# Kernel tuning notes

Hardware: AMD Instinct MI355X
Metric: run time of the kernel (lower is better)

Reference implementation:

```python
import jax, jax.numpy as jnp
import numpy as np

NUM_NEIGHBORS = 17
RATE = 0.5
BN_EPS = 1e-5
NEG_SLOPE = 0.1


def _neighbor_mask(n):
    # clamp branch (use_full_fov=False): mask[i, clamp(i+w, 0, n-1)] = 1 for w in [-k, k]
    half = NUM_NEIGHBORS // 2
    rows = np.arange(n)[:, None]
    cols = np.clip(rows + np.arange(-half, half + 1)[None, :], 0, n - 1)
    mask = np.zeros((n, n), dtype=np.float32)
    mask[np.repeat(np.arange(n), NUM_NEIGHBORS), cols.reshape(-1)] = 1.0
    return jnp.asarray(mask)


def _features(x, conv_w, conv_b, bn_gamma, bn_beta, bn_mean, bn_var):
    # conv kernel spans full length L with padding 0 -> a single dot per cutout
    # x: [B, N, C, L], conv_w: [H, C, L] -> [B, N, H]
    h = jnp.einsum('bncl,hcl->bnh', x, conv_w) + conv_b
    h = (h - bn_mean) * (bn_gamma / jnp.sqrt(bn_var + BN_EPS)) + bn_beta  # eval-mode BN1d
    return jnp.where(h >= 0, h, NEG_SLOPE * h)  # LeakyReLU(0.1)


def setup_inputs() -> dict:
    key = jax.random.key(0)
    ks = jax.random.split(key, 4)
    B, N, C, L, H = 8, 2048, 1, 56, 128
    return {
        'input': jax.random.normal(ks[0], (B, N, C, L), dtype=jnp.float32),
        'state_memory': jax.random.normal(ks[1], (B, N, C, L), dtype=jnp.float32),
        'conv_w': jax.random.normal(ks[2], (H, C, L), dtype=jnp.float32) * (2.0 / (C * L)) ** 0.5,
        'conv_b': jax.random.normal(ks[3], (H,), dtype=jnp.float32) * 0.02,
        'bn_gamma': jnp.ones((H,), dtype=jnp.float32),
        'bn_beta': jnp.zeros((H,), dtype=jnp.float32),
        'bn_mean': jnp.zeros((H,), dtype=jnp.float32),
        'bn_var': jnp.ones((H,), dtype=jnp.float32),
    }


def reference(input, state_memory, conv_w, conv_b, bn_gamma, bn_beta, bn_mean, bn_var):
    B, N, C, L = input.shape
    mask = _neighbor_mask(N)  # [N, N]

    f_in = _features(input, conv_w, conv_b, bn_gamma, bn_beta, bn_mean, bn_var)          # [B,N,H]
    f_mem = _features(state_memory, conv_w, conv_b, bn_gamma, bn_beta, bn_mean, bn_var)  # [B,N,H]

    sim = jnp.einsum('bnh,bmh->bnm', f_in, f_mem)      # [B,N,N]
    sim = sim - 1e10 * (1.0 - mask)
    sim_max = jnp.max(sim, axis=-1, keepdims=True)
    exps = jnp.exp(sim - sim_max) * mask
    attn = exps / jnp.sum(exps, axis=-1, keepdims=True)

    mem_flat = state_memory.reshape(B, N, C * L)
    attn_mem = jnp.einsum('bnm,bmd->bnd', attn, mem_flat).reshape(B, N, C, L)

    return RATE * input + (1.0 - RATE) * attn_mem
```

## Files before the change

### kernel.cpp

```cpp
#include <hip/hip_runtime.h>
#include <math.h>

#define NPTS   2048
#define LFEAT  56
#define HFEAT  128
#define HALFW  8
#define NEIGH  17
#define BR     32
#define BAND   48
#define LDW    132

__global__ __launch_bounds__(512) void fused_kernel(
    const float* __restrict__ x_in, const float* __restrict__ x_mem,
    const float* __restrict__ conv_w, const float* __restrict__ conv_b,
    const float* __restrict__ gamma,  const float* __restrict__ beta,
    const float* __restrict__ bmean,  const float* __restrict__ bvar,
    float* __restrict__ out, int R)
{
    __shared__ float4 xm4[BAND * 14];
    __shared__ float4 xi4[BR * 14];
    __shared__ float  fm[BAND][LDW];
    __shared__ float  fi[BR][LDW];

    const int tid    = threadIdx.x;
    const int chunks = NPTS / BR;
    const int b      = blockIdx.x / chunks;
    const int c0     = (blockIdx.x - b * chunks) * BR;
    const int bbase  = b * NPTS;

    const float4* srcm = (const float4*)(x_mem + (long)bbase * LFEAT);
    for (int i = tid; i < BAND * 14; i += 512) {
        const int r = i / 14, q = i - r * 14;
        const int g = min(max(c0 - HALFW + r, 0), NPTS - 1);
        xm4[i] = srcm[g * 14 + q];
    }
    const float4* srci = (const float4*)(x_in + (long)(bbase + c0) * LFEAT);
    for (int i = tid; i < BR * 14; i += 512) xi4[i] = srci[i];

    const int h  = tid & 127;
    const int rg = tid >> 7;
    float4 w4[14];
    #pragma unroll
    for (int q = 0; q < 14; ++q)
        w4[q] = ((const float4*)(conv_w + h * LFEAT))[q];
    const float sc = gamma[h] / sqrtf(bvar[h] + 1e-5f);
    const float sh = (conv_b[h] - bmean[h]) * sc + beta[h];

    __syncthreads();

    for (int r = rg; r < BAND; r += 4) {
        const float4* xr = &xm4[r * 14];
        float a0 = 0.0f, a1 = 0.0f;
        #pragma unroll
        for (int q = 0; q < 14; q += 2) {
            const float4 xa = xr[q], xb = xr[q + 1];
            a0 = fmaf(xa.x, w4[q].x, a0);     a0 = fmaf(xa.y, w4[q].y, a0);
            a0 = fmaf(xa.z, w4[q].z, a0);     a0 = fmaf(xa.w, w4[q].w, a0);
            a1 = fmaf(xb.x, w4[q + 1].x, a1); a1 = fmaf(xb.y, w4[q + 1].y, a1);
            a1 = fmaf(xb.z, w4[q + 1].z, a1); a1 = fmaf(xb.w, w4[q + 1].w, a1);
        }
        float f = (a0 + a1) * sc + sh;
        fm[r][h] = (f >= 0.0f) ? f : 0.1f * f;
    }
    for (int r = rg; r < BR; r += 4) {
        const float4* xr = &xi4[r * 14];
        float a0 = 0.0f, a1 = 0.0f;
        #pragma unroll
        for (int q = 0; q < 14; q += 2) {
            const float4 xa = xr[q], xb = xr[q + 1];
            a0 = fmaf(xa.x, w4[q].x, a0);     a0 = fmaf(xa.y, w4[q].y, a0);
            a0 = fmaf(xa.z, w4[q].z, a0);     a0 = fmaf(xa.w, w4[q].w, a0);
            a1 = fmaf(xb.x, w4[q + 1].x, a1); a1 = fmaf(xb.y, w4[q + 1].y, a1);
            a1 = fmaf(xb.z, w4[q + 1].z, a1); a1 = fmaf(xb.w, w4[q + 1].w, a1);
        }
        float f = (a0 + a1) * sc + sh;
        fi[r][h] = (f >= 0.0f) ? f : 0.1f * f;
    }
    __syncthreads();

    const int wave = tid >> 6;
    const int lane = tid & 63;
    const int lh   = lane & 31;
    const float* xmf = (const float*)xm4;
    const float* xif = (const float*)xi4;

    #pragma unroll
    for (int rr = 0; rr < 4; rr += 2) {
        const int l0   = wave * 4 + rr;
        const int lrow = l0 + (lane >> 5);
        const int n    = c0 + lrow;

        const int  mw    = n - HALFW + lh;
        const int  mc    = min(max(mw, 0), NPTS - 1);
        const int  slot  = mc - c0 + HALFW;
        const bool valid = (lh < NEIGH) && (mw >= 0) && (mw < NPTS);

        float p = -1e30f;
        if (lh < NEIGH) {
            const float4* a  = (const float4*)&fi[lrow][0];
            const float4* bb = (const float4*)&fm[slot][0];
            float4 A0 = {0.f,0.f,0.f,0.f}, A1 = {0.f,0.f,0.f,0.f};
            #pragma unroll
            for (int q = 0; q < 32; q += 2) {
                const float4 u0 = a[q],     v0 = bb[q];
                const float4 u1 = a[q + 1], v1 = bb[q + 1];
                A0.x = fmaf(u0.x, v0.x, A0.x); A0.y = fmaf(u0.y, v0.y, A0.y);
                A0.z = fmaf(u0.z, v0.z, A0.z); A0.w = fmaf(u0.w, v0.w, A0.w);
                A1.x = fmaf(u1.x, v1.x, A1.x); A1.y = fmaf(u1.y, v1.y, A1.y);
                A1.z = fmaf(u1.z, v1.z, A1.z); A1.w = fmaf(u1.w, v1.w, A1.w);
            }
            const float d = ((A0.x + A0.y) + (A0.z + A0.w))
                          + ((A1.x + A1.y) + (A1.z + A1.w));
            p = valid ? d : -1e30f;
        }

        float mx = p;
        #pragma unroll
        for (int off = 16; off >= 1; off >>= 1)
            mx = fmaxf(mx, __shfl_xor(mx, off));
        const float e = expf(p - mx);
        float sum = e;
        #pragma unroll
        for (int off = 16; off >= 1; off >>= 1)
            sum += __shfl_xor(sum, off);
        const float pn = e / sum;

        float swA[NEIGH], swB[NEIGH];
        #pragma unroll
        for (int w = 0; w < NEIGH; ++w) {
            swA[w] = __shfl(pn, w);
            swB[w] = __shfl(pn, 32 + w);
        }

        if (lane < LFEAT) {
            float accA = 0.0f, accB = 0.0f;
            #pragma unroll
            for (int w = 0; w < NEIGH; ++w) {
                const int sA = min(max(c0 + l0     - HALFW + w, 0), NPTS - 1) - c0 + HALFW;
                const int sB = min(max(c0 + l0 + 1 - HALFW + w, 0), NPTS - 1) - c0 + HALFW;
                accA = fmaf(swA[w], xmf[sA * LFEAT + lane], accA);
                accB = fmaf(swB[w], xmf[sB * LFEAT + lane], accB);
            }
            const long oA = (long)(bbase + c0 + l0) * LFEAT + lane;
            out[oA]         = 0.5f * xif[ l0      * LFEAT + lane] + 0.5f * accA;
            out[oA + LFEAT] = 0.5f * xif[(l0 + 1) * LFEAT + lane] + 0.5f * accB;
        }
    }
}

extern "C" void kernel_launch(void* const* d_in, const int* in_sizes, int n_in,
                              void* d_out, int out_size, void* d_ws, size_t ws_size,
                              hipStream_t stream)
{
    const float* input  = (const float*)d_in[0];
    const float* smem   = (const float*)d_in[1];
    const float* conv_w = (const float*)d_in[2];
    const float* conv_b = (const float*)d_in[3];
    const float* gamma  = (const float*)d_in[4];
    const float* beta   = (const float*)d_in[5];
    const float* bmean  = (const float*)d_in[6];
    const float* bvar   = (const float*)d_in[7];
    float* out = (float*)d_out;

    const int R = in_sizes[0] / LFEAT;
    const int blocks = (R / NPTS) * (NPTS / BR);

    fused_kernel<<<blocks, 512, 0, stream>>>(input, smem, conv_w, conv_b,
                                             gamma, beta, bmean, bvar, out, R);
}
```

Measured before the change: 101.4 us.

## Compute conv features from per-lane global loads broadcast with shuffles

The feature stage no longer reads the staged LDS rows. Each wave loads one 56-float row from global memory into lanes, prefetches the next row, and broadcasts elements with __shfl for the dot product against the register-held conv weights. The x_in LDS staging buffer and the first __syncthreads are removed, and the residual term now reads x_in from global directly. The aim is to drop a barrier and an LDS buffer, at the cost of many more cross-lane shuffle operations and exposed global-load latency in a non-unrolled loop. x_mem rows are also now read twice, once into LDS and once into registers.

```diff
diff --git a/kernel.cpp b/kernel.cpp
--- a/kernel.cpp
+++ b/kernel.cpp
@@ -18,11 +18,12 @@
     float* __restrict__ out, int R)
 {
     __shared__ float4 xm4[BAND * 14];
-    __shared__ float4 xi4[BR * 14];
     __shared__ float  fm[BAND][LDW];
     __shared__ float  fi[BR][LDW];
 
     const int tid    = threadIdx.x;
+    const int wave   = tid >> 6;
+    const int lane   = tid & 63;
     const int chunks = NPTS / BR;
     const int b      = blockIdx.x / chunks;
     const int c0     = (blockIdx.x - b * chunks) * BR;
@@ -34,11 +35,8 @@
         const int g = min(max(c0 - HALFW + r, 0), NPTS - 1);
         xm4[i] = srcm[g * 14 + q];
     }
-    const float4* srci = (const float4*)(x_in + (long)(bbase + c0) * LFEAT);
-    for (int i = tid; i < BR * 14; i += 512) xi4[i] = srci[i];
 
-    const int h  = tid & 127;
-    const int rg = tid >> 7;
+    const int h = ((wave & 1) << 6) | lane;
     float4 w4[14];
     #pragma unroll
     for (int q = 0; q < 14; ++q)
@@ -46,43 +44,44 @@
     const float sc = gamma[h] / sqrtf(bvar[h] + 1e-5f);
     const float sh = (conv_b[h] - bmean[h]) * sc + beta[h];
 
-    __syncthreads();
+    const int r0 = wave >> 1;
 
-    for (int r = rg; r < BAND; r += 4) {
-        const float4* xr = &xm4[r * 14];
+    #define ROWPTR(r) ((r) < BAND \
+        ? x_mem + (long)(bbase + min(max(c0 - HALFW + (r), 0), NPTS - 1)) * LFEAT \
+        : x_in  + (long)(bbase + c0 + ((r) - BAND)) * LFEAT)
+
+    float xv = (lane < LFEAT) ? ROWPTR(r0)[lane] : 0.0f;
+    #pragma unroll 1
+    for (int k = 0; k < 20; ++k) {
+        const int r = r0 + 4 * k;
+        float xnext = 0.0f;
+        if (k < 19) {
+            const float* p = ROWPTR(r + 4);
+            xnext = (lane < LFEAT) ? p[lane] : 0.0f;
+        }
         float a0 = 0.0f, a1 = 0.0f;
         #pragma unroll
         for (int q = 0; q < 14; q += 2) {
-            const float4 xa = xr[q], xb = xr[q + 1];
-            a0 = fmaf(xa.x, w4[q].x, a0);     a0 = fmaf(xa.y, w4[q].y, a0);
-            a0 = fmaf(xa.z, w4[q].z, a0);     a0 = fmaf(xa.w, w4[q].w, a0);
-            a1 = fmaf(xb.x, w4[q + 1].x, a1); a1 = fmaf(xb.y, w4[q + 1].y, a1);
-            a1 = fmaf(xb.z, w4[q + 1].z, a1); a1 = fmaf(xb.w, w4[q + 1].w, a1);
+            a0 = fmaf(__shfl(xv, 4*q + 0), w4[q].x, a0);
+            a0 = fmaf(__shfl(xv, 4*q + 1), w4[q].y, a0);
+            a0 = fmaf(__shfl(xv, 4*q + 2), w4[q].z, a0);
+            a0 = fmaf(__shfl(xv, 4*q + 3), w4[q].w, a0);
+            a1 = fmaf(__shfl(xv, 4*q + 4), w4[q+1].x, a1);
+            a1 = fmaf(__shfl(xv, 4*q + 5), w4[q+1].y, a1);
+            a1 = fmaf(__shfl(xv, 4*q + 6), w4[q+1].z, a1);
+            a1 = fmaf(__shfl(xv, 4*q + 7), w4[q+1].w, a1);
         }
         float f = (a0 + a1) * sc + sh;
-        fm[r][h] = (f >= 0.0f) ? f : 0.1f * f;
+        f = (f >= 0.0f) ? f : 0.1f * f;
+        if (r < BAND) fm[r][h] = f;
+        else          fi[r - BAND][h] = f;
+        xv = xnext;
     }
-    for (int r = rg; r < BR; r += 4) {
-        const float4* xr = &xi4[r * 14];
-        float a0 = 0.0f, a1 = 0.0f;
-        #pragma unroll
-        for (int q = 0; q < 14; q += 2) {
-            const float4 xa = xr[q], xb = xr[q + 1];
-            a0 = fmaf(xa.x, w4[q].x, a0);     a0 = fmaf(xa.y, w4[q].y, a0);
-            a0 = fmaf(xa.z, w4[q].z, a0);     a0 = fmaf(xa.w, w4[q].w, a0);
-            a1 = fmaf(xb.x, w4[q + 1].x, a1); a1 = fmaf(xb.y, w4[q + 1].y, a1);
-            a1 = fmaf(xb.z, w4[q + 1].z, a1); a1 = fmaf(xb.w, w4[q + 1].w, a1);
-        }
-        float f = (a0 + a1) * sc + sh;
-        fi[r][h] = (f >= 0.0f) ? f : 0.1f * f;
-    }
+    #undef ROWPTR
     __syncthreads();
 
-    const int wave = tid >> 6;
-    const int lane = tid & 63;
-    const int lh   = lane & 31;
+    const int lh = lane & 31;
     const float* xmf = (const float*)xm4;
-    const float* xif = (const float*)xi4;
 
     #pragma unroll
     for (int rr = 0; rr < 4; rr += 2) {
@@ -142,8 +141,8 @@
                 accB = fmaf(swB[w], xmf[sB * LFEAT + lane], accB);
             }
             const long oA = (long)(bbase + c0 + l0) * LFEAT + lane;
-            out[oA]         = 0.5f * xif[ l0      * LFEAT + lane] + 0.5f * accA;
-            out[oA + LFEAT] = 0.5f * xif[(l0 + 1) * LFEAT + lane] + 0.5f * accB;
+            out[oA]         = 0.5f * x_in[oA]         + 0.5f * accA;
+            out[oA + LFEAT] = 0.5f * x_in[oA + LFEAT] + 0.5f * accB;
         }
     }
 }
```

Result: slower. 135.0 us (+33.1%).
